# Optimization experiments

Hardware: AMD Instinct MI355X
Metric: run time of the kernel (lower is better)

The kernel has to match this reference:

```python
import jax, jax.numpy as jnp
import numpy as np

TEMPERATURE = 0.07
BASE_TEMPERATURE = 0.07
C = 0.01            # hyperbolic curvature (forward default)
ALPHA_D = 0.5       # distance-loss weight (forward default)

BSZ, N_VIEWS, DIM = 2048, 2, 256
N_CLASSES = 100


def setup_inputs() -> dict:
    key = jax.random.key(0)
    k1, k2 = jax.random.split(key)
    # features already live in the Poincare ball of curvature c=0.01 (radius 10);
    # scaled normals keep norms comfortably inside the ball.
    features = jax.random.normal(k1, (BSZ, N_VIEWS, DIM), dtype=jnp.float32) * 0.05
    labels = jax.random.randint(k2, (BSZ,), 0, N_CLASSES)
    return {"features": features, "labels": labels}


def _pairwise_mobius_dist(f, sq, gram, c):
    # norm of mobius_add(-x_i, x_j, c), computed analytically from inner products
    # (same math as materializing the NxNxD diff tensor, without the O(N^2 D) memory).
    # a = -x_i, b = x_j  =>  <a,b> = -gram, |a|^2 = sq_i, |b|^2 = sq_j
    a2 = sq[:, None]          # [N,1]
    b2 = sq[None, :]          # [1,N]
    ab = -gram                # [N,N]
    A = 1.0 + 2.0 * c * ab + c * b2
    B = 1.0 - c * a2
    den = 1.0 + 2.0 * c * ab + (c * c) * a2 * b2
    num_sq = A * A * a2 + 2.0 * A * B * ab + B * B * b2
    return jnp.sqrt(jnp.maximum(num_sq, 1e-12)) / den


def reference(features, labels) -> jnp.ndarray:
    bsz, n_views, dim = features.shape
    n = bsz * n_views
    f = features.reshape(n, dim)                       # [N,D]

    gram = f @ f.T                                     # [N,N]
    sq = jnp.sum(f * f, axis=-1)                       # [N]

    dists = _pairwise_mobius_dist(f, sq, gram, C)      # [N,N]
    sqrt_c = C ** 0.5
    dist_sim = (-2.0 / sqrt_c) * jnp.arctanh(jnp.minimum(sqrt_c * dists, 1.0 - 1e-5))

    inv_norm = jax.lax.rsqrt(jnp.maximum(sq, 1e-24))   # F.normalize
    ang_sim = gram * inv_norm[:, None] * inv_norm[None, :]

    sim = (ALPHA_D * dist_sim + (1.0 - ALPHA_D) * ang_sim) / TEMPERATURE
    logits = sim - jax.lax.stop_gradient(jnp.max(sim, axis=1, keepdims=True))

    pos_mask = (labels[:, None] == labels[None, :]).astype(jnp.float32)  # [bsz,bsz]
    pos_mask = jnp.tile(pos_mask, (n_views, n_views))                    # [N,N]
    logits_mask = 1.0 - jnp.eye(n, dtype=jnp.float32)                    # drop self
    pos_mask = pos_mask * logits_mask

    exp_logits = jnp.exp(logits) * logits_mask
    log_prob = logits - jnp.log(jnp.sum(exp_logits, axis=1, keepdims=True) + 1e-10)

    pos_pairs = jnp.sum(pos_mask, axis=1)
    pos_pairs = jnp.where(pos_pairs < 1e-6, 1.0, pos_pairs)
    mean_log_prob_pos = jnp.sum(pos_mask * log_prob, axis=1) / pos_pairs

    loss = -(TEMPERATURE / BASE_TEMPERATURE) * mean_log_prob_pos
    return loss.reshape(n_views, bsz).mean()
```

## Files before the change

### kernel.cpp

```cpp
#include <hip/hip_runtime.h>
#include <math.h>

#define NTOT 4096
#define BSZH 2048
#define DIMK 256
#define GY   32

typedef __bf16 bf16x8 __attribute__((ext_vector_type(8)));
typedef __bf16 bf16x4 __attribute__((ext_vector_type(4)));
typedef float  f32x4  __attribute__((ext_vector_type(4)));

__global__ __launch_bounds__(256) void k_prep(const float* __restrict__ f,
                                              __bf16* __restrict__ fbf,
                                              float* __restrict__ sq,
                                              float* __restrict__ out) {
    if (blockIdx.x == 0 && threadIdx.x == 0) out[0] = 0.0f;
    int row  = blockIdx.x * 4 + (threadIdx.x >> 6);
    int lane = threadIdx.x & 63;
    float4 v = *(const float4*)(f + row * DIMK + lane * 4);
    bf16x4 pk;
    pk[0] = (__bf16)v.x; pk[1] = (__bf16)v.y; pk[2] = (__bf16)v.z; pk[3] = (__bf16)v.w;
    int p = row >> 4, rr = row & 15, g = lane >> 1, half = lane & 1;
    *(bf16x4*)(fbf + (size_t)(p * 32 + g) * 128 + rr * 8 + half * 4) = pk;
    float s = v.x*v.x + v.y*v.y + v.z*v.z + v.w*v.w;
    #pragma unroll
    for (int off = 32; off > 0; off >>= 1) s += __shfl_xor(s, off, 64);
    if (lane == 0) sq[row] = s;
}

__global__ __launch_bounds__(256) void k_main(const __bf16* __restrict__ fbf,
                                              const int* __restrict__ labels,
                                              const float* __restrict__ sq,
                                              float4* __restrict__ part) {
    const int tid = threadIdx.x;
    const int wid = tid >> 6, lane = tid & 63;
    const int l15 = lane & 15, lg = lane >> 4;
    const int wr  = wid >> 1,  wc = wid & 1;
    const int bx = blockIdx.x, by = blockIdx.y;
    const int trow = bx * 128, tcol = by * 128;
    const int rowpan = bx * 8 + wr * 4;
    const int colpan = by * 8 + wc * 4;

    const char* base = (const char*)fbf + lane * 16;
    const char* ap[4]; const char* bp[4];
    #pragma unroll
    for (int i = 0; i < 4; ++i) {
        ap[i] = base + (size_t)(rowpan + i) * 8192;
        bp[i] = base + (size_t)(colpan + i) * 8192;
    }

    f32x4 acc[4][4];
    #pragma unroll
    for (int i = 0; i < 4; ++i)
        #pragma unroll
        for (int j = 0; j < 4; ++j) acc[i][j] = (f32x4){0.f, 0.f, 0.f, 0.f};

#define LDA(A_, B_, S) { \
    _Pragma("unroll") for (int i = 0; i < 4; ++i) { \
        A_[i] = *(const bf16x8*)(ap[i] + (S) * 1024); \
        B_[i] = *(const bf16x8*)(bp[i] + (S) * 1024); } }
#define FMA(A_, B_) { \
    _Pragma("unroll") for (int i = 0; i < 4; ++i) \
    _Pragma("unroll") for (int j = 0; j < 4; ++j) \
        acc[i][j] = __builtin_amdgcn_mfma_f32_16x16x32_bf16(A_[i], B_[j], acc[i][j], 0, 0, 0); }

    bf16x8 aA[4], bA[4], aB[4], bB[4];
    LDA(aA, bA, 0);
    LDA(aB, bB, 1); FMA(aA, bA);
    LDA(aA, bA, 2); FMA(aB, bB);
    LDA(aB, bB, 3); FMA(aA, bA);
    LDA(aA, bA, 4); FMA(aB, bB);
    LDA(aB, bB, 5); FMA(aA, bA);
    LDA(aA, bA, 6); FMA(aB, bB);
    LDA(aB, bB, 7); FMA(aA, bA);
    FMA(aB, bB);
#undef LDA
#undef FMA

    float cb2[4], cb2p[4], cb01[4], cinv[4]; int clab[4], ccol[4];
    #pragma unroll
    for (int j = 0; j < 4; ++j) {
        int col = tcol + wc * 64 + j * 16 + l15;
        float b2 = sq[col];
        ccol[j] = col; cb2[j] = b2;
        cb2p[j] = fmaf(0.01f, b2, 1.0f);
        cb01[j] = 0.01f * b2;
        cinv[j] = __builtin_amdgcn_rsqf(fmaxf(b2, 1e-24f));
        clab[j] = labels[col & (BSZH - 1)];
    }

    __shared__ float redR[2][2][64][3];

    #pragma unroll
    for (int i = 0; i < 4; ++i) {
        float rT[4], rP[4], rN[4];
        float ra2[4], rinv[4], Bv[4], B2v[4]; int rlab[4], rrow[4];
        #pragma unroll
        for (int t = 0; t < 4; ++t) {
            rT[t] = 0.f; rP[t] = 0.f; rN[t] = 0.f;
            int row = trow + wr * 64 + i * 16 + lg * 4 + t;
            float a2 = sq[row];
            rrow[t] = row; ra2[t] = a2;
            rinv[t] = __builtin_amdgcn_rsqf(fmaxf(a2, 1e-24f));
            rlab[t] = labels[row & (BSZH - 1)];
            float B = fmaf(-0.01f, a2, 1.0f);
            Bv[t] = B; B2v[t] = B * B;
        }
        #pragma unroll
        for (int j = 0; j < 4; ++j) {
            f32x4 a = acc[i][j];
            #pragma unroll
            for (int t = 0; t < 4; ++t) {
                float g   = a[t];
                float A   = fmaf(-0.02f, g, cb2p[j]);
                float den = fmaf(-cb01[j], Bv[t], A);
                float AB  = A * Bv[t];
                float num = fmaf(ra2[t] * A, A, fmaf(-(g + g), AB, cb2[j] * B2v[t]));
                float s   = __builtin_amdgcn_sqrtf(fmaxf(num, 1e-12f));
                float h   = 0.1f * s;
                float r   = (den + h) * __builtin_amdgcn_rcpf(den - h);
                float ang = g * rinv[t] * cinv[j];
                float tq  = fmaf(-71.4285714f, __builtin_amdgcn_logf(r), 10.3058781f * ang);
                float e   = __builtin_amdgcn_exp2f(tq);
                bool  dg  = (rrow[t] == ccol[j]);
                bool  pos = (!dg) && (rlab[t] == clab[j]);
                rT[t] += dg ? 0.f : e;
                rP[t] += pos ? 0.69314718f * tq : 0.f;
                rN[t] += pos ? 1.f : 0.f;
            }
        }
        #pragma unroll
        for (int t = 0; t < 4; ++t) {
            float T = rT[t], Pp = rP[t], Nn = rN[t];
            #pragma unroll
            for (int m = 1; m < 16; m <<= 1) {
                T  += __shfl_xor(T,  m, 64);
                Pp += __shfl_xor(Pp, m, 64);
                Nn += __shfl_xor(Nn, m, 64);
            }
            if (l15 == 0) {
                int rl = i * 16 + lg * 4 + t;
                redR[wr][wc][rl][0] = T; redR[wr][wc][rl][1] = Pp; redR[wr][wc][rl][2] = Nn;
            }
        }
    }
    __syncthreads();
    if (tid < 128) {
        int w = tid >> 6, rl = tid & 63;
        float T  = redR[w][0][rl][0] + redR[w][1][rl][0];
        float Pp = redR[w][0][rl][1] + redR[w][1][rl][1];
        float Nn = redR[w][0][rl][2] + redR[w][1][rl][2];
        part[(size_t)(trow + w * 64 + rl) * GY + by] = make_float4(T, Pp, Nn, 0.f);
    }
}

__global__ void k_final(const float4* __restrict__ part, float* __restrict__ out) {
    int row = blockIdx.x * 256 + threadIdx.x;
    float T = 0.f, P = 0.f, N = 0.f;
    #pragma unroll
    for (int k = 0; k < GY; ++k) {
        float4 p = part[(size_t)row * GY + k];
        T += p.x; P += p.y; N += p.z;
    }
    float v = (N < 1e-6f) ? 0.f
            : (__logf(T + 1.265037e-7f) - P / N) * (1.0f / NTOT);
    #pragma unroll
    for (int off = 32; off > 0; off >>= 1) v += __shfl_xor(v, off, 64);
    __shared__ float wsum[4];
    int wd = threadIdx.x >> 6, lane = threadIdx.x & 63;
    if (lane == 0) wsum[wd] = v;
    __syncthreads();
    if (threadIdx.x == 0) atomicAdd(out, wsum[0] + wsum[1] + wsum[2] + wsum[3]);
}

extern "C" void kernel_launch(void* const* d_in, const int* in_sizes, int n_in,
                              void* d_out, int out_size, void* d_ws, size_t ws_size,
                              hipStream_t stream) {
    const float* f      = (const float*)d_in[0];
    const int*   labels = (const int*)d_in[1];
    float* out = (float*)d_out;

    __bf16* fbf  = (__bf16*)d_ws;
    float*  sq   = (float*)((char*)d_ws + (size_t)NTOT * DIMK * 2);
    float4* part = (float4*)((char*)d_ws + (size_t)NTOT * DIMK * 2 + 65536);

    k_prep <<<dim3(NTOT / 4), dim3(256), 0, stream>>>(f, fbf, sq, out);
    k_main <<<dim3(GY, GY),   dim3(256), 0, stream>>>(fbf, labels, sq, part);
    k_final<<<dim3(NTOT / 256), dim3(256), 0, stream>>>(part, out);
}
```

Baseline: 98.52 us.

## Restage prep via LDS, simplify main loop, add occupancy hint, transpose partials

k_prep now handles one 16-row panel per block: it converts rows to bf16 into shared memory and writes the panel back with fully coalesced 16-byte stores. k_main drops the manual double-buffered load schedule in favour of a plain unrolled loop and adds a launch bound of 4 blocks per CU to cap register use. The diagonal test becomes a compile-time tile test instead of per-element row and column comparisons. Partials are stored column-major so k_final reads them coalesced. Capping registers and leaving load overlap to the compiler could cause spills or more exposed load latency.

```diff
diff --git a/kernel.cpp b/kernel.cpp
--- a/kernel.cpp
+++ b/kernel.cpp
@@ -7,7 +7,6 @@
 #define GY   32
 
 typedef __bf16 bf16x8 __attribute__((ext_vector_type(8)));
-typedef __bf16 bf16x4 __attribute__((ext_vector_type(4)));
 typedef float  f32x4  __attribute__((ext_vector_type(4)));
 
 __global__ __launch_bounds__(256) void k_prep(const float* __restrict__ f,
@@ -15,23 +14,40 @@
                                               float* __restrict__ sq,
                                               float* __restrict__ out) {
     if (blockIdx.x == 0 && threadIdx.x == 0) out[0] = 0.0f;
-    int row  = blockIdx.x * 4 + (threadIdx.x >> 6);
-    int lane = threadIdx.x & 63;
-    float4 v = *(const float4*)(f + row * DIMK + lane * 4);
-    bf16x4 pk;
-    pk[0] = (__bf16)v.x; pk[1] = (__bf16)v.y; pk[2] = (__bf16)v.z; pk[3] = (__bf16)v.w;
-    int p = row >> 4, rr = row & 15, g = lane >> 1, half = lane & 1;
-    *(bf16x4*)(fbf + (size_t)(p * 32 + g) * 128 + rr * 8 + half * 4) = pk;
-    float s = v.x*v.x + v.y*v.y + v.z*v.z + v.w*v.w;
+    const int tid   = threadIdx.x;
+    const int panel = blockIdx.x;
+    const int r  = tid >> 4;
+    const int gg = tid & 15;
+    __shared__ __align__(16) __bf16 lp[4096];
+
+    float s = 0.f;
     #pragma unroll
-    for (int off = 32; off > 0; off >>= 1) s += __shfl_xor(s, off, 64);
-    if (lane == 0) sq[row] = s;
+    for (int h = 0; h < 2; ++h) {
+        int g = gg + h * 16;
+        const float* src = f + (size_t)(panel * 16 + r) * DIMK + g * 8;
+        float4 v0 = *(const float4*)(src);
+        float4 v1 = *(const float4*)(src + 4);
+        s += v0.x*v0.x + v0.y*v0.y + v0.z*v0.z + v0.w*v0.w
+           + v1.x*v1.x + v1.y*v1.y + v1.z*v1.z + v1.w*v1.w;
+        bf16x8 pk;
+        pk[0] = (__bf16)v0.x; pk[1] = (__bf16)v0.y; pk[2] = (__bf16)v0.z; pk[3] = (__bf16)v0.w;
+        pk[4] = (__bf16)v1.x; pk[5] = (__bf16)v1.y; pk[6] = (__bf16)v1.z; pk[7] = (__bf16)v1.w;
+        *(bf16x8*)(lp + g * 128 + r * 8) = pk;
+    }
+    #pragma unroll
+    for (int m = 1; m < 16; m <<= 1) s += __shfl_xor(s, m, 64);
+    if (gg == 0) sq[panel * 16 + r] = s;
+    __syncthreads();
+    const bf16x8* srcv = (const bf16x8*)lp;
+    bf16x8* dst = (bf16x8*)(fbf + (size_t)panel * 4096);
+    dst[tid]       = srcv[tid];
+    dst[tid + 256] = srcv[tid + 256];
 }
 
-__global__ __launch_bounds__(256) void k_main(const __bf16* __restrict__ fbf,
-                                              const int* __restrict__ labels,
-                                              const float* __restrict__ sq,
-                                              float4* __restrict__ part) {
+__global__ __launch_bounds__(256, 4) void k_main(const __bf16* __restrict__ fbf,
+                                                 const int* __restrict__ labels,
+                                                 const float* __restrict__ sq,
+                                                 float4* __restrict__ part) {
     const int tid = threadIdx.x;
     const int wid = tid >> 6, lane = tid & 63;
     const int l15 = lane & 15, lg = lane >> 4;
@@ -40,14 +56,9 @@
     const int trow = bx * 128, tcol = by * 128;
     const int rowpan = bx * 8 + wr * 4;
     const int colpan = by * 8 + wc * 4;
+    const bool tilediag = (bx == by) && (wr == wc);
 
     const char* base = (const char*)fbf + lane * 16;
-    const char* ap[4]; const char* bp[4];
-    #pragma unroll
-    for (int i = 0; i < 4; ++i) {
-        ap[i] = base + (size_t)(rowpan + i) * 8192;
-        bp[i] = base + (size_t)(colpan + i) * 8192;
-    }
 
     f32x4 acc[4][4];
     #pragma unroll
@@ -55,34 +66,27 @@
         #pragma unroll
         for (int j = 0; j < 4; ++j) acc[i][j] = (f32x4){0.f, 0.f, 0.f, 0.f};
 
-#define LDA(A_, B_, S) { \
-    _Pragma("unroll") for (int i = 0; i < 4; ++i) { \
-        A_[i] = *(const bf16x8*)(ap[i] + (S) * 1024); \
-        B_[i] = *(const bf16x8*)(bp[i] + (S) * 1024); } }
-#define FMA(A_, B_) { \
-    _Pragma("unroll") for (int i = 0; i < 4; ++i) \
-    _Pragma("unroll") for (int j = 0; j < 4; ++j) \
-        acc[i][j] = __builtin_amdgcn_mfma_f32_16x16x32_bf16(A_[i], B_[j], acc[i][j], 0, 0, 0); }
+    #pragma unroll
+    for (int s = 0; s < 8; ++s) {
+        bf16x8 av[4], bv[4];
+        #pragma unroll
+        for (int i = 0; i < 4; ++i) {
+            av[i] = *(const bf16x8*)(base + (size_t)(rowpan + i) * 8192 + s * 1024);
+            bv[i] = *(const bf16x8*)(base + (size_t)(colpan + i) * 8192 + s * 1024);
+        }
+        #pragma unroll
+        for (int i = 0; i < 4; ++i)
+            #pragma unroll
+            for (int j = 0; j < 4; ++j)
+                acc[i][j] = __builtin_amdgcn_mfma_f32_16x16x32_bf16(av[i], bv[j], acc[i][j], 0, 0, 0);
+    }
 
-    bf16x8 aA[4], bA[4], aB[4], bB[4];
-    LDA(aA, bA, 0);
-    LDA(aB, bB, 1); FMA(aA, bA);
-    LDA(aA, bA, 2); FMA(aB, bB);
-    LDA(aB, bB, 3); FMA(aA, bA);
-    LDA(aA, bA, 4); FMA(aB, bB);
-    LDA(aB, bB, 5); FMA(aA, bA);
-    LDA(aA, bA, 6); FMA(aB, bB);
-    LDA(aB, bB, 7); FMA(aA, bA);
-    FMA(aB, bB);
-#undef LDA
-#undef FMA
-
-    float cb2[4], cb2p[4], cb01[4], cinv[4]; int clab[4], ccol[4];
+    float cb2[4], cb2p[4], cb01[4], cinv[4]; int clab[4];
     #pragma unroll
     for (int j = 0; j < 4; ++j) {
         int col = tcol + wc * 64 + j * 16 + l15;
         float b2 = sq[col];
-        ccol[j] = col; cb2[j] = b2;
+        cb2[j]  = b2;
         cb2p[j] = fmaf(0.01f, b2, 1.0f);
         cb01[j] = 0.01f * b2;
         cinv[j] = __builtin_amdgcn_rsqf(fmaxf(b2, 1e-24f));
@@ -94,13 +98,13 @@
     #pragma unroll
     for (int i = 0; i < 4; ++i) {
         float rT[4], rP[4], rN[4];
-        float ra2[4], rinv[4], Bv[4], B2v[4]; int rlab[4], rrow[4];
+        float ra2[4], rinv[4], Bv[4], B2v[4]; int rlab[4];
         #pragma unroll
         for (int t = 0; t < 4; ++t) {
             rT[t] = 0.f; rP[t] = 0.f; rN[t] = 0.f;
             int row = trow + wr * 64 + i * 16 + lg * 4 + t;
             float a2 = sq[row];
-            rrow[t] = row; ra2[t] = a2;
+            ra2[t]  = a2;
             rinv[t] = __builtin_amdgcn_rsqf(fmaxf(a2, 1e-24f));
             rlab[t] = labels[row & (BSZH - 1)];
             float B = fmaf(-0.01f, a2, 1.0f);
@@ -116,13 +120,13 @@
                 float den = fmaf(-cb01[j], Bv[t], A);
                 float AB  = A * Bv[t];
                 float num = fmaf(ra2[t] * A, A, fmaf(-(g + g), AB, cb2[j] * B2v[t]));
-                float s   = __builtin_amdgcn_sqrtf(fmaxf(num, 1e-12f));
-                float h   = 0.1f * s;
+                float sdt = __builtin_amdgcn_sqrtf(fmaxf(num, 1e-12f));
+                float h   = 0.1f * sdt;
                 float r   = (den + h) * __builtin_amdgcn_rcpf(den - h);
                 float ang = g * rinv[t] * cinv[j];
                 float tq  = fmaf(-71.4285714f, __builtin_amdgcn_logf(r), 10.3058781f * ang);
                 float e   = __builtin_amdgcn_exp2f(tq);
-                bool  dg  = (rrow[t] == ccol[j]);
+                bool  dg  = tilediag && (i == j) && (l15 == lg * 4 + t);
                 bool  pos = (!dg) && (rlab[t] == clab[j]);
                 rT[t] += dg ? 0.f : e;
                 rP[t] += pos ? 0.69314718f * tq : 0.f;
@@ -150,7 +154,7 @@
         float T  = redR[w][0][rl][0] + redR[w][1][rl][0];
         float Pp = redR[w][0][rl][1] + redR[w][1][rl][1];
         float Nn = redR[w][0][rl][2] + redR[w][1][rl][2];
-        part[(size_t)(trow + w * 64 + rl) * GY + by] = make_float4(T, Pp, Nn, 0.f);
+        part[(size_t)by * NTOT + trow + w * 64 + rl] = make_float4(T, Pp, Nn, 0.f);
     }
 }
 
@@ -159,7 +163,7 @@
     float T = 0.f, P = 0.f, N = 0.f;
     #pragma unroll
     for (int k = 0; k < GY; ++k) {
-        float4 p = part[(size_t)row * GY + k];
+        float4 p = part[(size_t)k * NTOT + row];
         T += p.x; P += p.y; N += p.z;
     }
     float v = (N < 1e-6f) ? 0.f
@@ -184,7 +188,7 @@
     float*  sq   = (float*)((char*)d_ws + (size_t)NTOT * DIMK * 2);
     float4* part = (float4*)((char*)d_ws + (size_t)NTOT * DIMK * 2 + 65536);
 
-    k_prep <<<dim3(NTOT / 4), dim3(256), 0, stream>>>(f, fbf, sq, out);
-    k_main <<<dim3(GY, GY),   dim3(256), 0, stream>>>(fbf, labels, sq, part);
+    k_prep <<<dim3(NTOT / 16), dim3(256), 0, stream>>>(f, fbf, sq, out);
+    k_main <<<dim3(GY, GY),    dim3(256), 0, stream>>>(fbf, labels, sq, part);
     k_final<<<dim3(NTOT / 256), dim3(256), 0, stream>>>(part, out);
 }
```

New measurement: 94.12 us. -4.5%, faster.
